# Kernel optimization log

Measured on AMD Instinct MI355X. Metric: run time of the kernel, lower is better.

The kernel has to match this reference:

```python
import jax, jax.numpy as jnp
import numpy as np

# Problem sizes (see shape_source): 32 point clouds of 2048 points each.
B, P, K = 32, 2048, 20
DIN, H, OUT = 3, 128, 128
N = B * P
EPS = 1e-5  # BatchNorm eps (eval mode: running stats mean=0, var=1)


def setup_inputs() -> dict:
    key = jax.random.key(0)
    ks = jax.random.split(key, 8)
    x = jax.random.normal(ks[0], (N, DIN), dtype=jnp.float32)
    batch = (jnp.arange(N) // P).astype(jnp.int32)  # equal-size clouds

    def lin(k, i, o):
        return (jax.random.normal(k, (i, o), dtype=jnp.float32) / np.sqrt(i)).astype(jnp.float32)

    return {
        "x": x, "batch": batch,
        # transfer = MLP([input_dim, hid_dim]) -> single Linear
        "Wt": lin(ks[1], DIN, H), "bt": jnp.zeros((H,), jnp.float32),
        # GINConv layer 0: Linear(H,2H) -> ReLU -> Linear(2H,H)
        "W1_0": lin(ks[2], H, 2 * H), "b1_0": jnp.zeros((2 * H,), jnp.float32),
        "W2_0": lin(ks[3], 2 * H, H), "b2_0": jnp.zeros((H,), jnp.float32),
        "g0": jnp.ones((H,), jnp.float32), "be0": jnp.zeros((H,), jnp.float32),
        "rm0": jnp.zeros((H,), jnp.float32), "rv0": jnp.ones((H,), jnp.float32),
        # GINConv layer 1
        "W1_1": lin(ks[4], H, 2 * H), "b1_1": jnp.zeros((2 * H,), jnp.float32),
        "W2_1": lin(ks[5], 2 * H, OUT), "b2_1": jnp.zeros((OUT,), jnp.float32),
        "g1": jnp.ones((OUT,), jnp.float32), "be1": jnp.zeros((OUT,), jnp.float32),
        "rm1": jnp.zeros((OUT,), jnp.float32), "rv1": jnp.ones((OUT,), jnp.float32),
    }


def _knn_idx(x):
    """Per-cloud kNN (includes self, dist 0), returns global neighbor ids [N,K]."""
    xb = x.reshape(B, P, DIN)
    sq = jnp.sum(xb * xb, axis=-1)  # [B,P]
    # squared euclidean distance [B,P,P]
    dist = sq[:, :, None] + sq[:, None, :] - 2.0 * jnp.einsum('bpd,bqd->bpq', xb, xb)
    _, idx = jax.lax.top_k(-dist, K)  # [B,P,K] nearest (incl. self)
    offs = (jnp.arange(B, dtype=idx.dtype) * P)[:, None, None]
    return (idx + offs).reshape(N, K)


def _bn_eval(h, g, be, rm, rv):
    return g * (h - rm) * jax.lax.rsqrt(rv + EPS) + be


def _gin_max(h, nbr, W1, b1, W2, b2):
    # max-aggregation over kNN neighbors + self loop, then GIN MLP
    agg = jnp.maximum(jnp.max(h[nbr], axis=1), h)  # [N,d]
    return jax.nn.relu(agg @ W1 + b1) @ W2 + b2


def reference(x, batch, Wt, bt,
              W1_0, b1_0, W2_0, b2_0, g0, be0, rm0, rv0,
              W1_1, b1_1, W2_1, b2_1, g1, be1, rm1, rv1):
    nbr = _knn_idx(jax.lax.stop_gradient(x))  # knn(x, x, k, batch).flip([0])
    h = x @ Wt + bt  # transfer MLP (single Linear)
    # layer 0: GINConv(max) -> BN -> ReLU (dropout identity in eval)
    h = _gin_max(h, nbr, W1_0, b1_0, W2_0, b2_0)
    h = jax.nn.relu(_bn_eval(h, g0, be0, rm0, rv0))
    # layer 1 (last): GINConv(max) -> BN -> dropout (identity)
    h = _gin_max(h, nbr, W1_1, b1_1, W2_1, b2_1)
    h = _bn_eval(h, g1, be1, rm1, rv1)
    return h
```

## Files before the change

kernel.cpp:

```cpp
#include <hip/hip_runtime.h>

typedef unsigned int u32;
typedef unsigned short u16;
typedef unsigned long long u64;

#define NPTS 65536
#define PCLD 2048
#define KNN 20
#define HD 128
#define HD2 256

typedef __attribute__((ext_vector_type(8))) short bf16x8;
typedef __attribute__((ext_vector_type(4))) float f32x4;
typedef unsigned short us2 __attribute__((ext_vector_type(2)));

__device__ __forceinline__ u16 f2bf(float f) {
    u32 u = __float_as_uint(f);
    u32 r = (u + 0x7FFFu + ((u >> 16) & 1u)) >> 16;
    return (u16)r;
}
__device__ __forceinline__ u32 enc2(u32 b) {
    u32 s = (b >> 15) & 0x00010001u;
    return b ^ (s * 0x7FFFu) ^ 0x80008000u;
}
__device__ __forceinline__ u32 dec2(u32 e) {
    u32 s = ((~e) >> 15) & 0x00010001u;
    return e ^ (s * 0x7FFFu) ^ 0x80008000u;
}
__device__ __forceinline__ u32 max2(u32 a, u32 b) {
#if __has_builtin(__builtin_elementwise_max)
    us2 x, y; __builtin_memcpy(&x, &a, 4); __builtin_memcpy(&y, &b, 4);
    us2 r = __builtin_elementwise_max(x, y);
    u32 o; __builtin_memcpy(&o, &r, 4); return o;
#else
    u32 lo = ((a & 0xFFFFu) > (b & 0xFFFFu)) ? (a & 0xFFFFu) : (b & 0xFFFFu);
    u32 hi = ((a >> 16) > (b >> 16)) ? (a & 0xFFFF0000u) : (b & 0xFFFF0000u);
    return lo | hi;
#endif
}

__global__ __launch_bounds__(256) void prep_kernel(
    const float* __restrict__ W1_0, const float* __restrict__ W2_0,
    const float* __restrict__ W1_1, const float* __restrict__ W2_1,
    u16* __restrict__ W1_0T, u16* __restrict__ W2_0T,
    u16* __restrict__ W1_1T, u16* __restrict__ W2_1T) {
    int id = blockIdx.x * 256 + threadIdx.x;
    int m = id >> 15, e = id & 32767;
    if (m == 0)      { int n = e >> 7, k = e & 127; W1_0T[e] = f2bf(W1_0[k * 256 + n]); }
    else if (m == 1) { int n = e >> 8, k = e & 255; W2_0T[e] = f2bf(W2_0[k * 128 + n]); }
    else if (m == 2) { int n = e >> 7, k = e & 127; W1_1T[e] = f2bf(W1_1[k * 256 + n]); }
    else             { int n = e >> 8, k = e & 255; W2_1T[e] = f2bf(W2_1[k * 128 + n]); }
}

__global__ __launch_bounds__(256) void knn_kernel(const float* __restrict__ x,
                                                  u16* __restrict__ nbr) {
    __shared__ float4 pts[PCLD];
    const int cloud = blockIdx.x >> 3;
    const int qi = ((blockIdx.x & 7) << 8) + threadIdx.x;
    const float* xc = x + (u64)cloud * PCLD * 3;
    for (int t = threadIdx.x; t < PCLD; t += 256) {
        float a = xc[3 * t], b = xc[3 * t + 1], c = xc[3 * t + 2];
        float sq = __fadd_rn(__fadd_rn(__fmul_rn(a, a), __fmul_rn(b, b)), __fmul_rn(c, c));
        pts[t] = make_float4(a, b, c, sq);
    }
    __syncthreads();
    const float4 q = pts[qi];
    const float qx = q.x, qy = q.y, qz = q.z, qs = q.w;
    const int lane = threadIdx.x & 63;
    u64 list[KNN];
#pragma unroll
    for (int k = 0; k < KNN; ++k) list[k] = 0xFF800000FFFFFFFFull;
    float thr = __builtin_inff();

    for (int base = 0; base < PCLD; base += 64) {
        float4 cp = pts[base + lane];
        u64 mask = 0;
#pragma unroll
        for (int c = 0; c < 64; ++c) {
            float cx = __uint_as_float(__builtin_amdgcn_readlane(__float_as_uint(cp.x), c));
            float cy = __uint_as_float(__builtin_amdgcn_readlane(__float_as_uint(cp.y), c));
            float cz = __uint_as_float(__builtin_amdgcn_readlane(__float_as_uint(cp.z), c));
            float cs = __uint_as_float(__builtin_amdgcn_readlane(__float_as_uint(cp.w), c));
            float dot = __builtin_fmaf(cz, qz, __builtin_fmaf(cy, qy, __fmul_rn(cx, qx)));
            float d = __fsub_rn(__fadd_rn(qs, cs), __fmul_rn(2.0f, dot));
            if (d < thr) mask |= (1ull << c);
        }
        while (mask) {
            int c = __builtin_ctzll(mask);
            mask &= mask - 1;
            float4 p2 = pts[base + c];
            float dot = __builtin_fmaf(p2.z, qz, __builtin_fmaf(p2.y, qy, __fmul_rn(p2.x, qx)));
            float d = __fsub_rn(__fadd_rn(qs, p2.w), __fmul_rn(2.0f, dot));
            if (d < thr) {
                u32 ub = __float_as_uint(d);
                u32 e = (ub & 0x80000000u) ? ~ub : (ub | 0x80000000u);
                u64 key = (((u64)e) << 32) | (u32)(base + c);
#pragma unroll
                for (int k = 0; k < KNN; ++k) {
                    u64 lo = key < list[k] ? key : list[k];
                    u64 hi = key < list[k] ? list[k] : key;
                    list[k] = lo; key = hi;
                }
                u32 e19 = (u32)(list[KNN - 1] >> 32);
                u32 ud = (e19 & 0x80000000u) ? (e19 & 0x7FFFFFFFu) : ~e19;
                thr = __uint_as_float(ud);
            }
        }
    }
    u16* out = nbr + (u64)(cloud * PCLD + qi) * KNN;
#pragma unroll
    for (int k = 0; k < KNN; ++k) out[k] = (u16)(u32)list[k];
}

__global__ __launch_bounds__(256) void feat_kernel(const float* __restrict__ x,
                                                   const float* __restrict__ Wt,
                                                   const float* __restrict__ bt,
                                                   u16* __restrict__ h0e) {
    int gid = blockIdx.x * 256 + threadIdx.x;
    int i = gid >> 4;
    int g = gid & 15;
    int c0 = g << 3;
    float x0 = x[3 * i], x1 = x[3 * i + 1], x2 = x[3 * i + 2];
    u32 o[4];
#pragma unroll
    for (int j = 0; j < 8; j += 2) {
        int c = c0 + j;
        float a0 = bt[c]     + x0 * Wt[c]     + x1 * Wt[128 + c]     + x2 * Wt[256 + c];
        float a1 = bt[c + 1] + x0 * Wt[c + 1] + x1 * Wt[128 + c + 1] + x2 * Wt[256 + c + 1];
        o[j >> 1] = enc2(((u32)f2bf(a0)) | (((u32)f2bf(a1)) << 16));
    }
    uint4* dst = (uint4*)&h0e[(u64)i * HD + c0];
    *dst = make_uint4(o[0], o[1], o[2], o[3]);
}

template <int RELU_OUT, int OUT_F32>
__global__ __launch_bounds__(256) void gemm_kernel(
    const u16* __restrict__ he, const u16* __restrict__ nbr_,
    const u16* __restrict__ W1T, const float* __restrict__ b1,
    const u16* __restrict__ W2T, const float* __restrict__ b2,
    const float* __restrict__ g, const float* __restrict__ be,
    const float* __restrict__ rm, const float* __restrict__ rv,
    void* __restrict__ hout_v) {
    __shared__ u16 aggL[64][136];
    __shared__ u16 hidL[64][264];
    const int tid = threadIdx.x;
    const int b = blockIdx.x;
    const int xcd = b & 7, j = b >> 3;
    const int cloud = xcd + 8 * (j >> 5);
    const int tile = j & 31;
    const int R = cloud * PCLD + tile * 64;

    {
        const int r = tid >> 2, cg = tid & 3;
        const int grow = R + r;
        const u16* __restrict__ hrow = he + (u64)grow * HD + cg * 32;
        uint4 m0 = ((const uint4*)hrow)[0];
        uint4 m1 = ((const uint4*)hrow)[1];
        uint4 m2 = ((const uint4*)hrow)[2];
        uint4 m3 = ((const uint4*)hrow)[3];
        const u64* nb8 = (const u64*)(nbr_ + (u64)grow * KNN);
        u64 nq[5];
#pragma unroll
        for (int w = 0; w < 5; ++w) nq[w] = nb8[w];
        const u16* __restrict__ hcl = he + (u64)cloud * PCLD * HD + cg * 32;
#pragma unroll 4
        for (int t = 0; t < KNN; ++t) {
            int loc = (int)(nq[t >> 2] >> ((t & 3) * 16)) & (PCLD - 1);
            const uint4* vp = (const uint4*)(hcl + (u64)loc * HD);
            uint4 v0 = vp[0], v1 = vp[1], v2 = vp[2], v3 = vp[3];
            m0.x = max2(m0.x, v0.x); m0.y = max2(m0.y, v0.y);
            m0.z = max2(m0.z, v0.z); m0.w = max2(m0.w, v0.w);
            m1.x = max2(m1.x, v1.x); m1.y = max2(m1.y, v1.y);
            m1.z = max2(m1.z, v1.z); m1.w = max2(m1.w, v1.w);
            m2.x = max2(m2.x, v2.x); m2.y = max2(m2.y, v2.y);
            m2.z = max2(m2.z, v2.z); m2.w = max2(m2.w, v2.w);
            m3.x = max2(m3.x, v3.x); m3.y = max2(m3.y, v3.y);
            m3.z = max2(m3.z, v3.z); m3.w = max2(m3.w, v3.w);
        }
        u32* dst = (u32*)&aggL[r][cg * 32];
        dst[0] = dec2(m0.x); dst[1] = dec2(m0.y); dst[2] = dec2(m0.z); dst[3] = dec2(m0.w);
        dst[4] = dec2(m1.x); dst[5] = dec2(m1.y); dst[6] = dec2(m1.z); dst[7] = dec2(m1.w);
        dst[8] = dec2(m2.x); dst[9] = dec2(m2.y); dst[10] = dec2(m2.z); dst[11] = dec2(m2.w);
        dst[12] = dec2(m3.x); dst[13] = dec2(m3.y); dst[14] = dec2(m3.z); dst[15] = dec2(m3.w);
    }
    __syncthreads();

    const int wv = tid >> 6, lane = tid & 63;
    const int lr = lane & 15;
    const int lq = lane >> 4;

    {
        f32x4 acc[4][4];
#pragma unroll
        for (int i = 0; i < 4; ++i)
#pragma unroll
            for (int j2 = 0; j2 < 4; ++j2) acc[i][j2] = (f32x4)(0.0f);
        const int nb0 = wv * 64;
#pragma unroll
        for (int ks = 0; ks < 4; ++ks) {
            const int kcol = ks * 32 + lq * 8;
            bf16x8 af[4], bfr[4];
#pragma unroll
            for (int mt = 0; mt < 4; ++mt)
                af[mt] = *(const bf16x8*)&aggL[mt * 16 + lr][kcol];
#pragma unroll
            for (int nt = 0; nt < 4; ++nt)
                bfr[nt] = *(const bf16x8*)&W1T[(u64)(nb0 + nt * 16 + lr) * HD + kcol];
#pragma unroll
            for (int mt = 0; mt < 4; ++mt)
#pragma unroll
                for (int nt = 0; nt < 4; ++nt)
                    acc[mt][nt] = __builtin_amdgcn_mfma_f32_16x16x32_bf16(af[mt], bfr[nt], acc[mt][nt], 0, 0, 0);
        }
#pragma unroll
        for (int nt = 0; nt < 4; ++nt) {
            const int c = nb0 + nt * 16 + lr;
            const float bias = b1[c];
#pragma unroll
            for (int mt = 0; mt < 4; ++mt)
#pragma unroll
                for (int r2 = 0; r2 < 4; ++r2) {
                    float v = fmaxf(acc[mt][nt][r2] + bias, 0.0f);
                    hidL[mt * 16 + lq * 4 + r2][c] = f2bf(v);
                }
        }
    }
    __syncthreads();

    {
        f32x4 acc[4][2];
#pragma unroll
        for (int i = 0; i < 4; ++i) { acc[i][0] = (f32x4)(0.0f); acc[i][1] = (f32x4)(0.0f); }
        const int nb0 = wv * 32;
#pragma unroll
        for (int ks = 0; ks < 8; ++ks) {
            const int kcol = ks * 32 + lq * 8;
            bf16x8 af[4], bfr[2];
#pragma unroll
            for (int mt = 0; mt < 4; ++mt)
                af[mt] = *(const bf16x8*)&hidL[mt * 16 + lr][kcol];
#pragma unroll
            for (int nt = 0; nt < 2; ++nt)
                bfr[nt] = *(const bf16x8*)&W2T[(u64)(nb0 + nt * 16 + lr) * HD2 + kcol];
#pragma unroll
            for (int mt = 0; mt < 4; ++mt)
#pragma unroll
                for (int nt = 0; nt < 2; ++nt)
                    acc[mt][nt] = __builtin_amdgcn_mfma_f32_16x16x32_bf16(af[mt], bfr[nt], acc[mt][nt], 0, 0, 0);
        }
#pragma unroll
        for (int nt = 0; nt < 2; ++nt) {
            const int c = nb0 + nt * 16 + lr;
            const float bias = b2[c];
            const float sc = g[c] * (1.0f / sqrtf(rv[c] + 1e-5f));
            const float rmc = rm[c];
            const float bec = be[c];
#pragma unroll
            for (int mt = 0; mt < 4; ++mt)
#pragma unroll
                for (int r2 = 0; r2 < 4; ++r2) {
                    float v = acc[mt][nt][r2] + bias;
                    v = (v - rmc) * sc + bec;
                    if (RELU_OUT) v = fmaxf(v, 0.0f);
                    const int row = R + mt * 16 + lq * 4 + r2;
                    if (OUT_F32) {
                        ((float*)hout_v)[(u64)row * HD + c] = v;
                    } else {
                        u16 bb = f2bf(v);
                        u16 e = bb ^ ((bb & 0x8000u) ? (u16)0xFFFFu : (u16)0x8000u);
                        ((u16*)hout_v)[(u64)row * HD + c] = e;
                    }
                }
        }
    }
}

extern "C" void kernel_launch(void* const* d_in, const int* in_sizes, int n_in,
                              void* d_out, int out_size, void* d_ws, size_t ws_size,
                              hipStream_t stream) {
    const float* x    = (const float*)d_in[0];
    const float* Wt   = (const float*)d_in[2];
    const float* bt   = (const float*)d_in[3];
    const float* W1_0 = (const float*)d_in[4];
    const float* b1_0 = (const float*)d_in[5];
    const float* W2_0 = (const float*)d_in[6];
    const float* b2_0 = (const float*)d_in[7];
    const float* g0   = (const float*)d_in[8];
    const float* be0  = (const float*)d_in[9];
    const float* rm0  = (const float*)d_in[10];
    const float* rv0  = (const float*)d_in[11];
    const float* W1_1 = (const float*)d_in[12];
    const float* b1_1 = (const float*)d_in[13];
    const float* W2_1 = (const float*)d_in[14];
    const float* b2_1 = (const float*)d_in[15];
    const float* g1   = (const float*)d_in[16];
    const float* be1  = (const float*)d_in[17];
    const float* rm1  = (const float*)d_in[18];
    const float* rv1  = (const float*)d_in[19];

    char* ws = (char*)d_ws;
    u16* he0  = (u16*)ws;
    u16* he1  = (u16*)(ws + 16777216);
    u16* W10T = (u16*)(ws + 2 * 16777216);
    u16* W20T = W10T + 32768;
    u16* W11T = W20T + 32768;
    u16* W21T = W11T + 32768;
    u16* nbr  = (u16*)(ws + 2 * 16777216 + 4 * 65536);

    knn_kernel<<<256, 256, 0, stream>>>(x, nbr);
    prep_kernel<<<512, 256, 0, stream>>>(W1_0, W2_0, W1_1, W2_1, W10T, W20T, W11T, W21T);
    feat_kernel<<<4096, 256, 0, stream>>>(x, Wt, bt, he0);
    gemm_kernel<1, 0><<<1024, 256, 0, stream>>>(he0, nbr, W10T, b1_0, W20T, b2_0,
                                                g0, be0, rm0, rv0, he1);
    gemm_kernel<0, 1><<<1024, 256, 0, stream>>>(he1, nbr, W11T, b1_1, W21T, b2_1,
                                                g1, be1, rm1, rv1, d_out);
}
```

Before: 340.4 us.

## Split kNN candidate scan across two thread halves with shared threshold and merge

Each query is now handled by two threads, each scanning half of the cloud's candidates, and the block grows to 512 threads. After every 64-candidate chunk the two threads exchange their current 20th-best distances through shared memory, so each can prune with the tighter of the two. At the end the second half writes its sorted list to LDS and the first half merges it into its own with insertion. This doubles the parallelism of the kNN stage, which previously ran only 256 blocks of 256 threads. The cost is extra LDS traffic, the merge step, a much larger LDS footprint per block, and register pressure at 512 threads that may limit occupancy.

```diff
diff --git a/kernel.cpp b/kernel.cpp
--- a/kernel.cpp
+++ b/kernel.cpp
@@ -52,27 +52,36 @@
     else             { int n = e >> 8, k = e & 255; W2_1T[e] = f2bf(W2_1[k * 128 + n]); }
 }
 
-__global__ __launch_bounds__(256) void knn_kernel(const float* __restrict__ x,
+__global__ __launch_bounds__(512) void knn_kernel(const float* __restrict__ x,
                                                   u16* __restrict__ nbr) {
     __shared__ float4 pts[PCLD];
+    __shared__ u64 lists[KNN][256];
+    __shared__ float thrS[512];
+    const int tid = threadIdx.x;
     const int cloud = blockIdx.x >> 3;
-    const int qi = ((blockIdx.x & 7) << 8) + threadIdx.x;
+    const int ql = ((blockIdx.x & 7) << 8) + (tid & 255);
+    const int half = tid >> 8;
     const float* xc = x + (u64)cloud * PCLD * 3;
-    for (int t = threadIdx.x; t < PCLD; t += 256) {
+    thrS[tid] = __builtin_inff();
+    for (int t = tid; t < PCLD; t += 512) {
         float a = xc[3 * t], b = xc[3 * t + 1], c = xc[3 * t + 2];
         float sq = __fadd_rn(__fadd_rn(__fmul_rn(a, a), __fmul_rn(b, b)), __fmul_rn(c, c));
         pts[t] = make_float4(a, b, c, sq);
     }
     __syncthreads();
-    const float4 q = pts[qi];
+    volatile float* thrV = thrS;
+    const float4 q = pts[ql];
     const float qx = q.x, qy = q.y, qz = q.z, qs = q.w;
-    const int lane = threadIdx.x & 63;
+    const int lane = tid & 63;
     u64 list[KNN];
 #pragma unroll
     for (int k = 0; k < KNN; ++k) list[k] = 0xFF800000FFFFFFFFull;
     float thr = __builtin_inff();
-
-    for (int base = 0; base < PCLD; base += 64) {
+    float pthr = __builtin_inff();
+
+    const int cbeg = half << 10;
+    for (int base = cbeg; base < cbeg + 1024; base += 64) {
+        float gate = fminf(thr, pthr);
         float4 cp = pts[base + lane];
         u64 mask = 0;
 #pragma unroll
@@ -83,7 +92,7 @@
             float cs = __uint_as_float(__builtin_amdgcn_readlane(__float_as_uint(cp.w), c));
             float dot = __builtin_fmaf(cz, qz, __builtin_fmaf(cy, qy, __fmul_rn(cx, qx)));
             float d = __fsub_rn(__fadd_rn(qs, cs), __fmul_rn(2.0f, dot));
-            if (d < thr) mask |= (1ull << c);
+            if (d < gate) mask |= (1ull << c);
         }
         while (mask) {
             int c = __builtin_ctzll(mask);
@@ -91,7 +100,7 @@
             float4 p2 = pts[base + c];
             float dot = __builtin_fmaf(p2.z, qz, __builtin_fmaf(p2.y, qy, __fmul_rn(p2.x, qx)));
             float d = __fsub_rn(__fadd_rn(qs, p2.w), __fmul_rn(2.0f, dot));
-            if (d < thr) {
+            if (d < gate) {
                 u32 ub = __float_as_uint(d);
                 u32 e = (ub & 0x80000000u) ? ~ub : (ub | 0x80000000u);
                 u64 key = (((u64)e) << 32) | (u32)(base + c);
@@ -104,12 +113,33 @@
                 u32 e19 = (u32)(list[KNN - 1] >> 32);
                 u32 ud = (e19 & 0x80000000u) ? (e19 & 0x7FFFFFFFu) : ~e19;
                 thr = __uint_as_float(ud);
+                gate = fminf(thr, pthr);
             }
         }
-    }
-    u16* out = nbr + (u64)(cloud * PCLD + qi) * KNN;
-#pragma unroll
-    for (int k = 0; k < KNN; ++k) out[k] = (u16)(u32)list[k];
+        thrV[tid] = thr;
+        pthr = thrV[tid ^ 256];
+    }
+
+    if (half) {
+#pragma unroll
+        for (int k = 0; k < KNN; ++k) lists[k][tid & 255] = list[k];
+    }
+    __syncthreads();
+    if (!half) {
+#pragma unroll
+        for (int j = 0; j < KNN; ++j) {
+            u64 key = lists[j][tid];
+#pragma unroll
+            for (int k = 0; k < KNN; ++k) {
+                u64 lo = key < list[k] ? key : list[k];
+                u64 hi = key < list[k] ? list[k] : key;
+                list[k] = lo; key = hi;
+            }
+        }
+        u16* out = nbr + (u64)(cloud * PCLD + ql) * KNN;
+#pragma unroll
+        for (int k = 0; k < KNN; ++k) out[k] = (u16)(u32)list[k];
+    }
 }
 
 __global__ __launch_bounds__(256) void feat_kernel(const float* __restrict__ x,
@@ -307,7 +337,7 @@
     u16* W21T = W11T + 32768;
     u16* nbr  = (u16*)(ws + 2 * 16777216 + 4 * 65536);
 
-    knn_kernel<<<256, 256, 0, stream>>>(x, nbr);
+    knn_kernel<<<256, 512, 0, stream>>>(x, nbr);
     prep_kernel<<<512, 256, 0, stream>>>(W1_0, W2_0, W1_1, W2_1, W10T, W20T, W11T, W21T);
     feat_kernel<<<4096, 256, 0, stream>>>(x, Wt, bt, he0);
     gemm_kernel<1, 0><<<1024, 256, 0, stream>>>(he0, nbr, W10T, b1_0, W20T, b2_0,
```

Result: slower. 371.4 us (+9.1%).
